# Performance work log

Hardware: AMD Instinct MI355X
Metric: run time of the kernel (lower is better)

The kernel has to match this reference:

```python
import jax, jax.numpy as jnp
import numpy as np

B, IN_C, OUT_C, K, H, W = 8, 256, 256, 3, 128, 128
EPS = 1e-8
ACT_SCALE = np.sqrt(2.0).astype(np.float32)


def setup_inputs() -> dict:
    key = jax.random.key(0)
    k1, k2, k3 = jax.random.split(key, 3)
    return {
        "x": jax.random.normal(k1, (B, IN_C, H, W), dtype=jnp.float32),
        "code": jax.random.normal(k2, (B, IN_C), dtype=jnp.float32),
        "weight": jax.random.normal(k3, (OUT_C, IN_C, K, K), dtype=jnp.float32),
        "bias": jnp.zeros((OUT_C,), dtype=jnp.float32),
    }


def reference(x, code, weight, bias):
    b, in_c, h, w = x.shape
    out_c, _, k, _ = weight.shape
    wscale = np.float32(1.0 / np.sqrt(k * k * in_c))
    # Same memory reinterpretation as torch .view: (out_c,in_c,k,k) -> (1,k,k,in_c,out_c)
    wv = (weight * wscale).reshape(1, k, k, in_c, out_c)
    # modulate per-sample by code over input channels
    wm = wv * code[:, None, None, :, None]            # [b,k,k,in_c,out_c]
    # demodulate: norm over (k,k,in_c) per (b,out_c)
    norm = jnp.sqrt(jnp.sum(wm * wm, axis=(1, 2, 3)) + EPS)  # [b,out_c]
    wm = wm / norm[:, None, None, None, :]
    # reshape to grouped-conv kernel [b*out_c, in_c, k, k]
    wk = jnp.transpose(wm, (0, 4, 3, 1, 2)).reshape(b * out_c, in_c, k, k)
    xg = x.reshape(1, b * in_c, h, w)
    y = jax.lax.conv_general_dilated(
        xg, wk, window_strides=(1, 1),
        padding=[(k // 2, k // 2), (k // 2, k // 2)],
        feature_group_count=b,
        dimension_numbers=("NCHW", "OIHW", "NCHW"))
    y = y.reshape(b, out_c, h, w) + bias[None, :, None, None]
    # LeakyReLU(0.2) * sqrt(2)
    return jnp.where(y >= 0, y, 0.2 * y) * ACT_SCALE
```

## Files before the change

kernel.cpp:

```cpp
#include <hip/hip_runtime.h>
#include <hip/hip_bf16.h>


typedef __attribute__((ext_vector_type(8))) short short8;
typedef __attribute__((ext_vector_type(4))) float floatx4;
typedef __attribute__((ext_vector_type(4))) unsigned short ushort4_t;
typedef __bf16 bf16x8 __attribute__((ext_vector_type(8)));

#define B_    8
#define IC_   256
#define OC_   256
#define HW_   128
#define PIX_  (HW_*HW_)
#define RTOT  2304
#define WSCALE (1.0f/48.0f)

#define SWZ(row) ((((row) ^ ((row) >> 2)) & 3) << 3)

static __device__ __forceinline__ floatx4 mfma_bf16(short8 a, short8 b, floatx4 c) {
  return __builtin_amdgcn_mfma_f32_16x16x32_bf16(
      __builtin_bit_cast(bf16x8, a), __builtin_bit_cast(bf16x8, b), c, 0, 0, 0);
}

static __device__ __forceinline__ unsigned short f2bf(float f) {
  unsigned int u = __builtin_bit_cast(unsigned int, f);
  return (unsigned short)(u >> 16) + (unsigned short)((u >> 15) & 1u);
}

__global__ __launch_bounds__(256) void k_zero(float* __restrict__ p, int n) {
  int i = blockIdx.x * 256 + threadIdx.x;
  if (i < n) p[i] = 0.f;
}

__global__ __launch_bounds__(256) void k_transpose(const float* __restrict__ x,
                                                   unsigned short* __restrict__ Xt,
                                                   int b0) {
  __shared__ unsigned short t[64][66];
  const int tid = threadIdx.x;
  const int p0 = blockIdx.x * 64, ic0 = blockIdx.y * 64, bz = blockIdx.z;
  const float* xb = x + (size_t)(b0 + bz) * IC_ * PIX_;
  unsigned short* xtb = Xt + (size_t)bz * PIX_ * IC_;

  const int c2 = tid & 15, r2 = tid >> 4;
#pragma unroll
  for (int jr = 0; jr < 4; ++jr) {
    const int row = r2 + jr * 16;
    floatx4 f = *(const floatx4*)(&xb[(size_t)(ic0 + row) * PIX_ + p0 + 4 * c2]);
    ushort4_t w = { f2bf(f[0]), f2bf(f[1]), f2bf(f[2]), f2bf(f[3]) };
    *(ushort4_t*)(&t[row][4 * c2]) = w;
  }
  __syncthreads();
#pragma unroll
  for (int jj = 0; jj < 4; ++jj) {
    const int px = r2 + jj * 16;
    ushort4_t v = { t[4 * c2 + 0][px], t[4 * c2 + 1][px],
                    t[4 * c2 + 2][px], t[4 * c2 + 3][px] };
    *(ushort4_t*)(&xtb[(size_t)(p0 + px) * IC_ + ic0 + 4 * c2]) = v;
  }
}

__global__ __launch_bounds__(256) void k_norm(const float* __restrict__ Wraw,
                                              const float* __restrict__ code,
                                              float* __restrict__ norm2) {
  const int tap = blockIdx.x % 9, b = blockIdx.x / 9;
  const int oc = threadIdx.x;
  __shared__ float cs[IC_];
  cs[oc] = code[b * IC_ + oc];
  __syncthreads();
  float s = 0.f;
#pragma unroll 8
  for (int ic = 0; ic < IC_; ++ic) {
    float v = Wraw[(size_t)(tap * IC_ + ic) * OC_ + oc] * cs[ic];
    s += v * v;
  }
  atomicAdd(&norm2[b * OC_ + oc], s * (WSCALE * WSCALE));
}

__global__ __launch_bounds__(256) void k_modw(const float* __restrict__ Wraw,
                                              const float* __restrict__ code,
                                              const float* __restrict__ norm2,
                                              unsigned short* __restrict__ Wt) {
  const int idx = blockIdx.x * 256 + threadIdx.x;
  const int r  = idx % RTOT;
  const int t2 = idx / RTOT;
  const int oc = t2 & 255;
  const int b  = t2 >> 8;
  const int ic = r & 255;
  const float w  = Wraw[(size_t)r * OC_ + oc];
  const float cd = code[b * IC_ + ic];
  const float rn = rsqrtf(norm2[b * OC_ + oc] + 1e-8f);
  Wt[idx] = f2bf(w * cd * WSCALE * rn);
}

__global__ __launch_bounds__(256, 2) void k_conv(const unsigned short* __restrict__ Xt,
                                                 const unsigned short* __restrict__ Wt,
                                                 const float* __restrict__ bias,
                                                 float* __restrict__ out,
                                                 int b0) {
  __shared__ __align__(16) unsigned short Wl[2][3][128 * 32];
  __shared__ __align__(16) unsigned short Xl[2][130 * 32];

  const int tid  = threadIdx.x;
  const int lane = tid & 63;
  const int wv   = tid >> 6;
  const int wm   = wv & 1;
  const int wn   = wv >> 1;
  const int l15  = lane & 15;
  const int k0   = (lane >> 4) * 8;

  const int nwg  = (int)(gridDim.x * gridDim.y * gridDim.z);
  const int q    = nwg >> 3;
  const int flat = (int)(blockIdx.x + gridDim.x * (blockIdx.y + gridDim.y * blockIdx.z));
  const int nf   = (flat & 7) * q + (flat >> 3);
  const int py = nf & 127, ot = (nf >> 7) & 1, bz = nf >> 8;
  const int b  = b0 + bz;

  const unsigned short* Wtp = Wt + (size_t)(b * OC_ + ot * 128) * RTOT;
  const unsigned short* Xtp = Xt + (size_t)bz * PIX_ * IC_;

  const int xc   = 1 + (tid >> 1);
  const int xh   = tid & 1;
  const int wocr = tid >> 1;
  const int sST  = SWZ(wocr);
  const int sXC  = SWZ(xc);

  const int sA  = SWZ(l15);
  const int sB0 = SWZ(l15 + 0), sB1 = SWZ(l15 + 1), sB2 = SWZ(l15 + 2);

  const int lo = (py > 0) ? py - 1 : 0;
  const int hi = (py < HW_ - 1) ? py + 1 : HW_ - 1;
  const int NS = (hi - lo + 1) * 8;

  const floatx4 zz = {0.f, 0.f, 0.f, 0.f};
  floatx4 acc[4][4];
#pragma unroll
  for (int i = 0; i < 4; ++i)
#pragma unroll
    for (int j = 0; j < 4; ++j) acc[i][j] = zz;

  if (tid < 128) {
    const int bi = tid >> 6, rr = tid & 63;
    const int r = (rr < 32) ? 0 : 129;
    Xl[bi][r * 32 + (rr & 31)] = 0;
  }

  short8 xr0, xr1, wr0, wr1, wr2, wr3, wr4, wr5;

#define CLOAD(s_) do {                                                           \
    const int iy_   = lo + ((s_) >> 3);                                          \
    const int icc_  = (s_) & 7;                                                  \
    const int tapb_ = (iy_ - py + 1) * 3;                                        \
    const unsigned short* xs_ =                                                  \
        Xtp + (size_t)(iy_ * HW_ + xc - 1) * IC_ + icc_ * 32 + xh * 16;          \
    xr0 = *(const short8*)(xs_);                                                 \
    xr1 = *(const short8*)(xs_ + 8);                                             \
    const unsigned short* ws_ =                                                  \
        Wtp + (size_t)wocr * RTOT + (size_t)tapb_ * IC_ + icc_ * 32 + xh * 16;   \
    wr0 = *(const short8*)(ws_);                                                 \
    wr1 = *(const short8*)(ws_ + 8);                                             \
    wr2 = *(const short8*)(ws_ + IC_);                                           \
    wr3 = *(const short8*)(ws_ + IC_ + 8);                                       \
    wr4 = *(const short8*)(ws_ + 2 * IC_);                                       \
    wr5 = *(const short8*)(ws_ + 2 * IC_ + 8);                                   \
  } while (0)

#define DSW(b_) do {                                                             \
    unsigned short* xd_ = &Xl[b_][xc * 32];                                      \
    *(short8*)(&xd_[(xh * 16)     ^ sXC]) = xr0;                                 \
    *(short8*)(&xd_[(xh * 16 + 8) ^ sXC]) = xr1;                                 \
    unsigned short* wd0_ = &Wl[b_][0][wocr * 32];                                \
    unsigned short* wd1_ = &Wl[b_][1][wocr * 32];                                \
    unsigned short* wd2_ = &Wl[b_][2][wocr * 32];                                \
    *(short8*)(&wd0_[(xh * 16)     ^ sST]) = wr0;                                \
    *(short8*)(&wd0_[(xh * 16 + 8) ^ sST]) = wr1;                                \
    *(short8*)(&wd1_[(xh * 16)     ^ sST]) = wr2;                                \
    *(short8*)(&wd1_[(xh * 16 + 8) ^ sST]) = wr3;                                \
    *(short8*)(&wd2_[(xh * 16)     ^ sST]) = wr4;                                \
    *(short8*)(&wd2_[(xh * 16 + 8) ^ sST]) = wr5;                                \
  } while (0)

  CLOAD(0);
  DSW(0);
  __syncthreads();

  for (int s = 0; s < NS; ++s) {
    const int nb = s & 1;
    if (s + 1 < NS) CLOAD(s + 1);

    __builtin_amdgcn_s_setprio(1);
#pragma unroll
    for (int kx = 0; kx < 3; ++kx) {
      const int sB = (kx == 0) ? sB0 : (kx == 1) ? sB1 : sB2;
      short8 af[4], bfr[4];
#pragma unroll
      for (int i = 0; i < 4; ++i)
        af[i] = *(const short8*)(&Wl[nb][kx][(wm * 64 + i * 16 + l15) * 32 + (k0 ^ sA)]);
#pragma unroll
      for (int j = 0; j < 4; ++j)
        bfr[j] = *(const short8*)(&Xl[nb][(wn * 64 + j * 16 + l15 + kx) * 32 + (k0 ^ sB)]);
#pragma unroll
      for (int i = 0; i < 4; ++i)
#pragma unroll
        for (int j = 0; j < 4; ++j)
          acc[i][j] = mfma_bf16(af[i], bfr[j], acc[i][j]);
    }
    __builtin_amdgcn_s_setprio(0);

    if (s + 1 < NS) DSW(nb ^ 1);
    __syncthreads();
  }

#undef CLOAD
#undef DSW

  const int row0 = (lane >> 4) * 4;
#pragma unroll
  for (int i = 0; i < 4; ++i) {
#pragma unroll
    for (int p = 0; p < 4; ++p) {
      const int oc = ot * 128 + wm * 64 + i * 16 + row0 + p;
      const float bvf = bias[oc];
#pragma unroll
      for (int j = 0; j < 4; ++j) {
        const int px = wn * 64 + j * 16 + l15;
        float v = acc[i][j][p] + bvf;
        v = (v >= 0.f ? v : 0.2f * v) * 1.41421356237f;
        out[((size_t)(b * OC_ + oc) * HW_ + py) * HW_ + px] = v;
      }
    }
  }
}

extern "C" void kernel_launch(void* const* d_in, const int* in_sizes, int n_in,
                              void* d_out, int out_size, void* d_ws, size_t ws_size,
                              hipStream_t stream) {
  const float* x    = (const float*)d_in[0];
  const float* code = (const float*)d_in[1];
  const float* wgt  = (const float*)d_in[2];
  const float* bias = (const float*)d_in[3];

  const size_t WT_BYTES = (size_t)B_ * OC_ * RTOT * 2;
  const size_t N2_BYTES = (size_t)B_ * OC_ * 4;
  const size_t XT_OFF   = WT_BYTES + N2_BYTES;
  const size_t XB_BYTES = (size_t)PIX_ * IC_ * 2;

  unsigned short* Wt = (unsigned short*)d_ws;
  float* norm2       = (float*)((char*)d_ws + WT_BYTES);
  unsigned short* Xt = (unsigned short*)((char*)d_ws + XT_OFF);

  int bc = 8;
  while (bc > 1 && XT_OFF + (size_t)bc * XB_BYTES > ws_size) bc >>= 1;

  k_zero<<<(B_ * OC_ + 255) / 256, 256, 0, stream>>>(norm2, B_ * OC_);
  k_norm<<<B_ * 9, 256, 0, stream>>>(wgt, code, norm2);
  k_modw<<<(B_ * OC_ * RTOT) / 256, 256, 0, stream>>>(wgt, code, norm2, Wt);
  for (int b0 = 0; b0 < B_; b0 += bc) {
    k_transpose<<<dim3(PIX_ / 64, IC_ / 64, bc), 256, 0, stream>>>(x, Xt, b0);
    k_conv<<<dim3(HW_, 2, bc), 256, 0, stream>>>(Xt, Wt, bias, (float*)d_out, b0);
  }
}
```

Before: 424.8 us.

## Use 512-thread conv workgroups with eight waves over halved pixel tiles

Doubles the conv workgroup to 512 threads, so eight waves each compute a 64x32 output sub-tile instead of four waves computing 64x64. The cooperative global-to-LDS staging is redistributed so each thread loads one 16-byte X chunk and three weight chunks. The aim is to cut per-thread registers and raise wave-level parallelism for latency hiding. In exchange, each wave has less register reuse, issues more LDS reads per MFMA because the A fragments are reused over fewer B fragments, and there are more waves per barrier.

```diff
diff --git a/kernel.cpp b/kernel.cpp
--- a/kernel.cpp
+++ b/kernel.cpp
@@ -92,7 +92,7 @@
   Wt[idx] = f2bf(w * cd * WSCALE * rn);
 }
 
-__global__ __launch_bounds__(256, 2) void k_conv(const unsigned short* __restrict__ Xt,
+__global__ __launch_bounds__(512, 4) void k_conv(const unsigned short* __restrict__ Xt,
                                                  const unsigned short* __restrict__ Wt,
                                                  const float* __restrict__ bias,
                                                  float* __restrict__ out,
@@ -118,11 +118,10 @@
   const unsigned short* Wtp = Wt + (size_t)(b * OC_ + ot * 128) * RTOT;
   const unsigned short* Xtp = Xt + (size_t)bz * PIX_ * IC_;
 
-  const int xc   = 1 + (tid >> 1);
-  const int xh   = tid & 1;
-  const int wocr = tid >> 1;
-  const int sST  = SWZ(wocr);
-  const int sXC  = SWZ(xc);
+  const int srow = tid >> 2;
+  const int sq   = tid & 3;
+  const int sOffW = (sq * 8) ^ SWZ(srow);
+  const int sOffX = (sq * 8) ^ SWZ(srow + 1);
 
   const int sA  = SWZ(l15);
   const int sB0 = SWZ(l15 + 0), sB1 = SWZ(l15 + 1), sB2 = SWZ(l15 + 2);
@@ -132,11 +131,11 @@
   const int NS = (hi - lo + 1) * 8;
 
   const floatx4 zz = {0.f, 0.f, 0.f, 0.f};
-  floatx4 acc[4][4];
+  floatx4 acc[4][2];
 #pragma unroll
   for (int i = 0; i < 4; ++i)
 #pragma unroll
-    for (int j = 0; j < 4; ++j) acc[i][j] = zz;
+    for (int j = 0; j < 2; ++j) acc[i][j] = zz;
 
   if (tid < 128) {
     const int bi = tid >> 6, rr = tid & 63;
@@ -144,39 +143,27 @@
     Xl[bi][r * 32 + (rr & 31)] = 0;
   }
 
-  short8 xr0, xr1, wr0, wr1, wr2, wr3, wr4, wr5;
+  short8 xr0, wr0, wr1, wr2;
 
 #define CLOAD(s_) do {                                                           \
     const int iy_   = lo + ((s_) >> 3);                                          \
     const int icc_  = (s_) & 7;                                                  \
     const int tapb_ = (iy_ - py + 1) * 3;                                        \
     const unsigned short* xs_ =                                                  \
-        Xtp + (size_t)(iy_ * HW_ + xc - 1) * IC_ + icc_ * 32 + xh * 16;          \
+        Xtp + (size_t)(iy_ * HW_ + srow) * IC_ + icc_ * 32 + sq * 8;             \
     xr0 = *(const short8*)(xs_);                                                 \
-    xr1 = *(const short8*)(xs_ + 8);                                             \
     const unsigned short* ws_ =                                                  \
-        Wtp + (size_t)wocr * RTOT + (size_t)tapb_ * IC_ + icc_ * 32 + xh * 16;   \
+        Wtp + (size_t)srow * RTOT + (size_t)tapb_ * IC_ + icc_ * 32 + sq * 8;    \
     wr0 = *(const short8*)(ws_);                                                 \
-    wr1 = *(const short8*)(ws_ + 8);                                             \
-    wr2 = *(const short8*)(ws_ + IC_);                                           \
-    wr3 = *(const short8*)(ws_ + IC_ + 8);                                       \
-    wr4 = *(const short8*)(ws_ + 2 * IC_);                                       \
-    wr5 = *(const short8*)(ws_ + 2 * IC_ + 8);                                   \
+    wr1 = *(const short8*)(ws_ + IC_);                                           \
+    wr2 = *(const short8*)(ws_ + 2 * IC_);                                       \
   } while (0)
 
 #define DSW(b_) do {                                                             \
-    unsigned short* xd_ = &Xl[b_][xc * 32];                                      \
-    *(short8*)(&xd_[(xh * 16)     ^ sXC]) = xr0;                                 \
-    *(short8*)(&xd_[(xh * 16 + 8) ^ sXC]) = xr1;                                 \
-    unsigned short* wd0_ = &Wl[b_][0][wocr * 32];                                \
-    unsigned short* wd1_ = &Wl[b_][1][wocr * 32];                                \
-    unsigned short* wd2_ = &Wl[b_][2][wocr * 32];                                \
-    *(short8*)(&wd0_[(xh * 16)     ^ sST]) = wr0;                                \
-    *(short8*)(&wd0_[(xh * 16 + 8) ^ sST]) = wr1;                                \
-    *(short8*)(&wd1_[(xh * 16)     ^ sST]) = wr2;                                \
-    *(short8*)(&wd1_[(xh * 16 + 8) ^ sST]) = wr3;                                \
-    *(short8*)(&wd2_[(xh * 16)     ^ sST]) = wr4;                                \
-    *(short8*)(&wd2_[(xh * 16 + 8) ^ sST]) = wr5;                                \
+    *(short8*)(&Xl[b_][(srow + 1) * 32 + sOffX])  = xr0;                         \
+    *(short8*)(&Wl[b_][0][srow * 32 + sOffW])     = wr0;                         \
+    *(short8*)(&Wl[b_][1][srow * 32 + sOffW])     = wr1;                         \
+    *(short8*)(&Wl[b_][2][srow * 32 + sOffW])     = wr2;                         \
   } while (0)
 
   CLOAD(0);
@@ -191,17 +178,17 @@
 #pragma unroll
     for (int kx = 0; kx < 3; ++kx) {
       const int sB = (kx == 0) ? sB0 : (kx == 1) ? sB1 : sB2;
-      short8 af[4], bfr[4];
+      short8 af[4], bfr[2];
 #pragma unroll
       for (int i = 0; i < 4; ++i)
         af[i] = *(const short8*)(&Wl[nb][kx][(wm * 64 + i * 16 + l15) * 32 + (k0 ^ sA)]);
 #pragma unroll
-      for (int j = 0; j < 4; ++j)
-        bfr[j] = *(const short8*)(&Xl[nb][(wn * 64 + j * 16 + l15 + kx) * 32 + (k0 ^ sB)]);
+      for (int j = 0; j < 2; ++j)
+        bfr[j] = *(const short8*)(&Xl[nb][(wn * 32 + j * 16 + l15 + kx) * 32 + (k0 ^ sB)]);
 #pragma unroll
       for (int i = 0; i < 4; ++i)
 #pragma unroll
-        for (int j = 0; j < 4; ++j)
+        for (int j = 0; j < 2; ++j)
           acc[i][j] = mfma_bf16(af[i], bfr[j], acc[i][j]);
     }
     __builtin_amdgcn_s_setprio(0);
@@ -221,8 +208,8 @@
       const int oc = ot * 128 + wm * 64 + i * 16 + row0 + p;
       const float bvf = bias[oc];
 #pragma unroll
-      for (int j = 0; j < 4; ++j) {
-        const int px = wn * 64 + j * 16 + l15;
+      for (int j = 0; j < 2; ++j) {
+        const int px = wn * 32 + j * 16 + l15;
         float v = acc[i][j][p] + bvf;
         v = (v >= 0.f ? v : 0.2f * v) * 1.41421356237f;
         out[((size_t)(b * OC_ + oc) * HW_ + py) * HW_ + px] = v;
@@ -256,6 +243,6 @@
   k_modw<<<(B_ * OC_ * RTOT) / 256, 256, 0, stream>>>(wgt, code, norm2, Wt);
   for (int b0 = 0; b0 < B_; b0 += bc) {
     k_transpose<<<dim3(PIX_ / 64, IC_ / 64, bc), 256, 0, stream>>>(x, Xt, b0);
-    k_conv<<<dim3(HW_, 2, bc), 256, 0, stream>>>(Xt, Wt, bias, (float*)d_out, b0);
-  }
-}
+    k_conv<<<dim3(HW_, 2, bc), 512, 0, stream>>>(Xt, Wt, bias, (float*)d_out, b0);
+  }
+}
```

New measurement: 431.0 us. About the same (+1.4%).

## Fuse input transpose and bf16 conversion into conv kernel load path

Applied to the files above, without the earlier changes.

Removes the separate transpose kernel that wrote a bf16 NHWC copy of x. The conv kernel now reads fp32 x directly in NCHW with 16 strided scalar loads per thread, converts to bf16 in registers and writes the transposed tile into LDS. The LDS swizzle pattern changes to match the new store layout. This drops a full write-and-reread of the activation tensor and several launches, but it costs more global load instructions, twice the bytes of x per load (fp32 instead of bf16), and x is re-read by both output-channel tiles and three rows.

```diff
diff --git a/kernel.cpp b/kernel.cpp
--- a/kernel.cpp
+++ b/kernel.cpp
@@ -4,7 +4,6 @@
 
 typedef __attribute__((ext_vector_type(8))) short short8;
 typedef __attribute__((ext_vector_type(4))) float floatx4;
-typedef __attribute__((ext_vector_type(4))) unsigned short ushort4_t;
 typedef __bf16 bf16x8 __attribute__((ext_vector_type(8)));
 
 #define B_    8
@@ -15,7 +14,7 @@
 #define RTOT  2304
 #define WSCALE (1.0f/48.0f)
 
-#define SWZ(row) ((((row) ^ ((row) >> 2)) & 3) << 3)
+#define SWZ(row) ((((row) >> 1) & 3) << 3)
 
 static __device__ __forceinline__ floatx4 mfma_bf16(short8 a, short8 b, floatx4 c) {
   return __builtin_amdgcn_mfma_f32_16x16x32_bf16(
@@ -30,33 +29,6 @@
 __global__ __launch_bounds__(256) void k_zero(float* __restrict__ p, int n) {
   int i = blockIdx.x * 256 + threadIdx.x;
   if (i < n) p[i] = 0.f;
-}
-
-__global__ __launch_bounds__(256) void k_transpose(const float* __restrict__ x,
-                                                   unsigned short* __restrict__ Xt,
-                                                   int b0) {
-  __shared__ unsigned short t[64][66];
-  const int tid = threadIdx.x;
-  const int p0 = blockIdx.x * 64, ic0 = blockIdx.y * 64, bz = blockIdx.z;
-  const float* xb = x + (size_t)(b0 + bz) * IC_ * PIX_;
-  unsigned short* xtb = Xt + (size_t)bz * PIX_ * IC_;
-
-  const int c2 = tid & 15, r2 = tid >> 4;
-#pragma unroll
-  for (int jr = 0; jr < 4; ++jr) {
-    const int row = r2 + jr * 16;
-    floatx4 f = *(const floatx4*)(&xb[(size_t)(ic0 + row) * PIX_ + p0 + 4 * c2]);
-    ushort4_t w = { f2bf(f[0]), f2bf(f[1]), f2bf(f[2]), f2bf(f[3]) };
-    *(ushort4_t*)(&t[row][4 * c2]) = w;
-  }
-  __syncthreads();
-#pragma unroll
-  for (int jj = 0; jj < 4; ++jj) {
-    const int px = r2 + jj * 16;
-    ushort4_t v = { t[4 * c2 + 0][px], t[4 * c2 + 1][px],
-                    t[4 * c2 + 2][px], t[4 * c2 + 3][px] };
-    *(ushort4_t*)(&xtb[(size_t)(p0 + px) * IC_ + ic0 + 4 * c2]) = v;
-  }
 }
 
 __global__ __launch_bounds__(256) void k_norm(const float* __restrict__ Wraw,
@@ -92,11 +64,10 @@
   Wt[idx] = f2bf(w * cd * WSCALE * rn);
 }
 
-__global__ __launch_bounds__(256, 2) void k_conv(const unsigned short* __restrict__ Xt,
+__global__ __launch_bounds__(256, 2) void k_conv(const float* __restrict__ x,
                                                  const unsigned short* __restrict__ Wt,
                                                  const float* __restrict__ bias,
-                                                 float* __restrict__ out,
-                                                 int b0) {
+                                                 float* __restrict__ out) {
   __shared__ __align__(16) unsigned short Wl[2][3][128 * 32];
   __shared__ __align__(16) unsigned short Xl[2][130 * 32];
 
@@ -112,20 +83,20 @@
   const int q    = nwg >> 3;
   const int flat = (int)(blockIdx.x + gridDim.x * (blockIdx.y + gridDim.y * blockIdx.z));
   const int nf   = (flat & 7) * q + (flat >> 3);
-  const int py = nf & 127, ot = (nf >> 7) & 1, bz = nf >> 8;
-  const int b  = b0 + bz;
+  const int py = nf & 127, ot = (nf >> 7) & 1, b = nf >> 8;
 
   const unsigned short* Wtp = Wt + (size_t)(b * OC_ + ot * 128) * RTOT;
-  const unsigned short* Xtp = Xt + (size_t)bz * PIX_ * IC_;
-
-  const int xc   = 1 + (tid >> 1);
+  const float* xb = x + (size_t)b * IC_ * PIX_;
+
+  const int srow = tid >> 1;
   const int xh   = tid & 1;
-  const int wocr = tid >> 1;
-  const int sST  = SWZ(wocr);
-  const int sXC  = SWZ(xc);
+  const int sW   = SWZ(srow);
+  const int sX   = SWZ(srow + 1);
+  const int eW0  = (xh * 16) ^ sW;
+  const int eX0  = (xh * 16) ^ sX;
 
   const int sA  = SWZ(l15);
-  const int sB0 = SWZ(l15 + 0), sB1 = SWZ(l15 + 1), sB2 = SWZ(l15 + 2);
+  const int sB0 = SWZ(l15), sB1 = SWZ(l15 + 1), sB2 = SWZ(l15 + 2);
 
   const int lo = (py > 0) ? py - 1 : 0;
   const int hi = (py < HW_ - 1) ? py + 1 : HW_ - 1;
@@ -144,18 +115,18 @@
     Xl[bi][r * 32 + (rr & 31)] = 0;
   }
 
-  short8 xr0, xr1, wr0, wr1, wr2, wr3, wr4, wr5;
+  float xr[16];
+  short8 wr0, wr1, wr2, wr3, wr4, wr5;
 
 #define CLOAD(s_) do {                                                           \
     const int iy_   = lo + ((s_) >> 3);                                          \
     const int icc_  = (s_) & 7;                                                  \
     const int tapb_ = (iy_ - py + 1) * 3;                                        \
-    const unsigned short* xs_ =                                                  \
-        Xtp + (size_t)(iy_ * HW_ + xc - 1) * IC_ + icc_ * 32 + xh * 16;          \
-    xr0 = *(const short8*)(xs_);                                                 \
-    xr1 = *(const short8*)(xs_ + 8);                                             \
+    const float* xs_ = xb + (size_t)(icc_ * 32 + xh * 16) * PIX_ + iy_ * HW_ + srow; \
+    _Pragma("unroll")                                                            \
+    for (int i_ = 0; i_ < 16; ++i_) xr[i_] = xs_[(size_t)i_ * PIX_];             \
     const unsigned short* ws_ =                                                  \
-        Wtp + (size_t)wocr * RTOT + (size_t)tapb_ * IC_ + icc_ * 32 + xh * 16;   \
+        Wtp + (size_t)srow * RTOT + (size_t)tapb_ * IC_ + icc_ * 32 + xh * 16;   \
     wr0 = *(const short8*)(ws_);                                                 \
     wr1 = *(const short8*)(ws_ + 8);                                             \
     wr2 = *(const short8*)(ws_ + IC_);                                           \
@@ -165,18 +136,24 @@
   } while (0)
 
 #define DSW(b_) do {                                                             \
-    unsigned short* xd_ = &Xl[b_][xc * 32];                                      \
-    *(short8*)(&xd_[(xh * 16)     ^ sXC]) = xr0;                                 \
-    *(short8*)(&xd_[(xh * 16 + 8) ^ sXC]) = xr1;                                 \
-    unsigned short* wd0_ = &Wl[b_][0][wocr * 32];                                \
-    unsigned short* wd1_ = &Wl[b_][1][wocr * 32];                                \
-    unsigned short* wd2_ = &Wl[b_][2][wocr * 32];                                \
-    *(short8*)(&wd0_[(xh * 16)     ^ sST]) = wr0;                                \
-    *(short8*)(&wd0_[(xh * 16 + 8) ^ sST]) = wr1;                                \
-    *(short8*)(&wd1_[(xh * 16)     ^ sST]) = wr2;                                \
-    *(short8*)(&wd1_[(xh * 16 + 8) ^ sST]) = wr3;                                \
-    *(short8*)(&wd2_[(xh * 16)     ^ sST]) = wr4;                                \
-    *(short8*)(&wd2_[(xh * 16 + 8) ^ sST]) = wr5;                                \
+    short8 p0_, p1_;                                                             \
+    _Pragma("unroll")                                                            \
+    for (int c_ = 0; c_ < 8; ++c_) {                                             \
+      p0_[c_] = (short)f2bf(xr[c_]);                                             \
+      p1_[c_] = (short)f2bf(xr[8 + c_]);                                         \
+    }                                                                            \
+    unsigned short* xd_ = &Xl[b_][(srow + 1) * 32];                              \
+    *(short8*)(&xd_[eX0])     = p0_;                                             \
+    *(short8*)(&xd_[eX0 ^ 8]) = p1_;                                             \
+    unsigned short* wd0_ = &Wl[b_][0][srow * 32];                                \
+    unsigned short* wd1_ = &Wl[b_][1][srow * 32];                                \
+    unsigned short* wd2_ = &Wl[b_][2][srow * 32];                                \
+    *(short8*)(&wd0_[eW0])     = wr0;                                            \
+    *(short8*)(&wd0_[eW0 ^ 8]) = wr1;                                            \
+    *(short8*)(&wd1_[eW0])     = wr2;                                            \
+    *(short8*)(&wd1_[eW0 ^ 8]) = wr3;                                            \
+    *(short8*)(&wd2_[eW0])     = wr4;                                            \
+    *(short8*)(&wd2_[eW0 ^ 8]) = wr5;                                            \
   } while (0)
 
   CLOAD(0);
@@ -240,22 +217,12 @@
   const float* bias = (const float*)d_in[3];
 
   const size_t WT_BYTES = (size_t)B_ * OC_ * RTOT * 2;
-  const size_t N2_BYTES = (size_t)B_ * OC_ * 4;
-  const size_t XT_OFF   = WT_BYTES + N2_BYTES;
-  const size_t XB_BYTES = (size_t)PIX_ * IC_ * 2;
 
   unsigned short* Wt = (unsigned short*)d_ws;
   float* norm2       = (float*)((char*)d_ws + WT_BYTES);
-  unsigned short* Xt = (unsigned short*)((char*)d_ws + XT_OFF);
-
-  int bc = 8;
-  while (bc > 1 && XT_OFF + (size_t)bc * XB_BYTES > ws_size) bc >>= 1;
 
   k_zero<<<(B_ * OC_ + 255) / 256, 256, 0, stream>>>(norm2, B_ * OC_);
   k_norm<<<B_ * 9, 256, 0, stream>>>(wgt, code, norm2);
   k_modw<<<(B_ * OC_ * RTOT) / 256, 256, 0, stream>>>(wgt, code, norm2, Wt);
-  for (int b0 = 0; b0 < B_; b0 += bc) {
-    k_transpose<<<dim3(PIX_ / 64, IC_ / 64, bc), 256, 0, stream>>>(x, Xt, b0);
-    k_conv<<<dim3(HW_, 2, bc), 256, 0, stream>>>(Xt, Wt, bias, (float*)d_out, b0);
-  }
-}
+  k_conv<<<dim3(HW_, 2, B_), 256, 0, stream>>>(x, Wt, bias, (float*)d_out);
+}
```

After: 466.8 us. +9.9%, slower.
